# Kernel tuning notes

Hardware: AMD Instinct MI355X
Metric: run time of the kernel (lower is better)

Reference implementation:

```python
import jax, jax.numpy as jnp
import numpy as np
from jax import lax

INF = 1e10
R = 20          # max_distance: EDT truncated at this radius (exact under clamp)
NUM_CLASSES = 19


def _pass1d(f, axis):
    """1D squared distance transform min_{|d|<=R} (d^2 + f[shifted]), truncated.
    f: [..., H, W] with 0 at 'source' pixels, INF elsewhere. Out-of-bounds = INF
    (matches scipy, which sees nothing beyond the array border)."""
    pad = [(0, 0)] * f.ndim
    pad[axis] = (R, R)
    fp = jnp.pad(f, pad, constant_values=INF)
    n = f.shape[axis]
    out = jnp.full_like(f, INF)
    for d in range(2 * R + 1):  # fixed small loop (41 iters), jit-unrolled
        shifted = lax.slice_in_dim(fp, d, d + n, axis=axis)
        out = jnp.minimum(out, shifted + float((d - R) ** 2))
    return out


def edt_trunc(mask):
    """Euclidean distance from each True pixel to nearest False pixel,
    truncated at R (False pixels get 0). mask: [..., H, W] bool."""
    f = jnp.where(mask, INF, 0.0).astype(jnp.float32)
    g = _pass1d(f, -2)
    g = _pass1d(g, -1)
    return jnp.sqrt(jnp.minimum(g, float(R * R)))


def compute_sdf(onehot_bool):
    """Signed distance: negdist - posdist, per [B,C,H,W] one-hot masks.
    Already truncated at +-R, matching clamp(-R, R) in the torch module."""
    posdist = edt_trunc(onehot_bool)    # distance inside FG to BG
    negdist = edt_trunc(~onehot_bool)   # distance inside BG to FG
    return negdist - posdist


def setup_inputs() -> dict:
    key = jax.random.key(0)
    k1, k2 = jax.random.split(key)
    logits = jax.random.normal(k1, (8, NUM_CLASSES, 256, 512), dtype=jnp.float32)
    targets = jax.random.randint(k2, (8, 256, 512), 0, NUM_CLASSES, dtype=jnp.int64)
    return {"logits": logits, "targets": targets}


def reference(logits, targets):
    C = logits.shape[1]
    probs = jax.nn.softmax(logits, axis=1)                       # [B,C,H,W]
    onehot = jax.nn.one_hot(targets, C, axis=1, dtype=jnp.bool_)  # [B,C,H,W]
    sdf = compute_sdf(onehot)
    sdf = jnp.clip(sdf, -float(R), float(R)) / float(R)
    # mean over spatial, sum over classes, mean over batch (reduction='mean')
    per_class = jnp.mean(probs * sdf, axis=(2, 3))               # [B,C]
    loss = jnp.sum(per_class, axis=1)                            # [B]
    return jnp.mean(loss)
```

## Files before the change

kernel.cpp:

```cpp
#include <hip/hip_runtime.h>
#include <hip/hip_bf16.h>
#include <math.h>

#define NCLS 19
#define BB   8
#define HH   256
#define WW   512
#define CAP2 400u
#define SEG  4

typedef unsigned short u16x2 __attribute__((ext_vector_type(2)));

static __device__ __forceinline__ unsigned umin32(unsigned a, unsigned b) { return a < b ? a : b; }
static __device__ __forceinline__ float fsqrt_fast(float x) { return __builtin_amdgcn_sqrtf(x); }

static __device__ __forceinline__ unsigned pk_add_s(unsigned v, unsigned c) {
    unsigned d; asm("v_pk_add_u16 %0, %1, %2" : "=v"(d) : "s"(c), "v"(v)); return d;
}
static __device__ __forceinline__ unsigned pk_minv(unsigned a, unsigned b) {
    unsigned d; asm("v_pk_min_u16 %0, %1, %2" : "=v"(d) : "v"(a), "v"(b)); return d;
}
static __device__ __forceinline__ unsigned pk_maxv(unsigned a, unsigned b) {
    unsigned d; asm("v_pk_max_u16 %0, %1, %2" : "=v"(d) : "v"(a), "v"(b)); return d;
}
static __device__ __forceinline__ unsigned pk_hmin(unsigned a) {
    unsigned d;
    asm("v_pk_min_u16 %0, %1, %1 op_sel:[1,0] op_sel_hi:[0,1]" : "=v"(d) : "v"(a));
    return d;
}
static __device__ __forceinline__ void sq8(unsigned x, unsigned& w0, unsigned& w1) {
    unsigned a = x & 0x00FF00FFu;
    unsigned b = (x >> 8) & 0x00FF00FFu;
    u16x2 sa = __builtin_bit_cast(u16x2, a); sa = sa * sa;
    u16x2 sb = __builtin_bit_cast(u16x2, b); sb = sb * sb;
    unsigned ua = __builtin_bit_cast(unsigned, sa);
    unsigned ub = __builtin_bit_cast(unsigned, sb);
    w0 = __builtin_amdgcn_perm(ub, ua, 0x05040100u);
    w1 = __builtin_amdgcn_perm(ub, ua, 0x07060302u);
}

__global__ __launch_bounds__(256)
void kA_vert(const int* __restrict__ targ, unsigned char* __restrict__ vneg,
             unsigned long long* __restrict__ acc) {
    if (blockIdx.x == 0 && threadIdx.x == 0) { *acc = 0ULL; }
    int gid = blockIdx.x * 256 + threadIdx.x;
    int col = gid & 4095;
    int seg = gid >> 12;
    int b = col >> 9;
    int w = col & 511;
    int h0 = seg * SEG;
    const int* tp = &targ[b * HH * WW + w];

    unsigned d[NCLS], pk[NCLS];
#pragma unroll
    for (int c = 0; c < NCLS; ++c) { d[c] = 21u; pk[c] = 0u; }
#pragma unroll
    for (int k = 0; k < 21 + SEG; ++k) {
        int hh = h0 - 21 + k;
        int t = -1;
        if (hh >= 0) t = tp[hh * WW];
#pragma unroll
        for (int c = 0; c < NCLS; ++c)
            d[c] = (t == c) ? 0u : d[c] + 1u;
        if (k >= 21) {
            int r = k - 21;
#pragma unroll
            for (int c = 0; c < NCLS; ++c)
                pk[c] |= d[c] << (r * 8);
        }
    }
    unsigned u[NCLS];
#pragma unroll
    for (int c = 0; c < NCLS; ++c) u[c] = 21u;
#pragma unroll
    for (int k = 0; k < 21 + SEG; ++k) {
        int hh = h0 + SEG - 1 + 21 - k;
        int t = -1;
        if (hh < HH) t = tp[hh * WW];
#pragma unroll
        for (int c = 0; c < NCLS; ++c)
            u[c] = (t == c) ? 0u : u[c] + 1u;
        if (k >= 21) {
            int r = SEG - 1 - (k - 21);
#pragma unroll
            for (int c = 0; c < NCLS; ++c) {
                unsigned dv = (pk[c] >> (r * 8)) & 0xffu;
                vneg[((size_t)(b * NCLS + c) * HH + (h0 + r)) * WW + w] =
                    (unsigned char)umin32(dv, u[c]);
            }
        }
    }
}

__global__ __launch_bounds__(256)
void kB_main(const float* __restrict__ logits, const int* __restrict__ targ,
             const unsigned char* __restrict__ vneg,
             unsigned long long* __restrict__ acc) {
    __shared__ float sNum[4][256];
    __shared__ float sDen[4][256];
    __shared__ float sEt[4][256];
    __shared__ unsigned short sM2[4][256];
    __shared__ float wsum[4];
    int tid = threadIdx.x;
    int L = tid & 63;
    int wid = tid >> 6;
    int bh = blockIdx.x;
    int b = bh >> 8;
    int h = bh & 255;

    const unsigned HALO2 = 441u | (441u << 16);

#define SQx(x) ((unsigned)((x) * (x)))
#define PK2(a, bq) (SQx(a) | (SQx(bq) << 16))
    const unsigned CE[21] = {
        PK2(-20,-19), PK2(-18,-17), PK2(-16,-15), PK2(-14,-13), PK2(-12,-11),
        PK2(-10,-9),  PK2(-8,-7),   PK2(-6,-5),   PK2(-4,-3),   PK2(-2,-1),
        PK2(0,1),     PK2(2,3),     PK2(4,5),     PK2(6,7),     PK2(8,9),
        PK2(10,11),   PK2(12,13),   PK2(14,15),   PK2(16,17),   PK2(18,19),
        PK2(20,21) };
    const unsigned CO[21] = {
        PK2(-21,-20), PK2(-19,-18), PK2(-17,-16), PK2(-15,-14), PK2(-13,-12),
        PK2(-11,-10), PK2(-9,-8),   PK2(-7,-6),   PK2(-5,-4),   PK2(-3,-2),
        PK2(-1,0),    PK2(1,2),     PK2(3,4),     PK2(5,6),     PK2(7,8),
        PK2(9,10),    PK2(11,12),   PK2(13,14),   PK2(15,16),   PK2(17,18),
        PK2(19,20) };
#undef PK2
#undef SQx

    int im1 = ((L + 63) & 63) * 4, im2 = ((L + 62) & 63) * 4, im3 = ((L + 61) & 63) * 4;
    int ip1 = ((L + 1) & 63) * 4,  ip2 = ((L + 2) & 63) * 4,  ip3 = ((L + 3) & 63) * 4;

    const uint2* vrw = (const uint2*)vneg + ((size_t)(b * NCLS + wid) * HH + h) * 64 + L;
    const float* lroww = &logits[((size_t)(b * NCLS + wid) * HH + h) * WW + 8 * L];
    int nc = (wid < 3) ? 5 : 4;

    int t8[8];
    {
        const int4* tr = (const int4*)&targ[((size_t)b * HH + h) * WW + 8 * L];
        int4 ta = tr[0], tb = tr[1];
        t8[0]=ta.x; t8[1]=ta.y; t8[2]=ta.z; t8[3]=ta.w;
        t8[4]=tb.x; t8[5]=tb.y; t8[6]=tb.z; t8[7]=tb.w;
    }

    float den[8], num[8], et[8];
    unsigned m2[8];
#pragma unroll
    for (int p = 0; p < 8; ++p) { den[p]=0.f; num[p]=0.f; et[p]=0.f; m2[p]=0xFFFFu; }

    uint2 v8n = vrw[0];
    float4 f0n = *(const float4*)lroww;
    float4 f1n = *(const float4*)(lroww + 4);

#pragma unroll 1
    for (int i = 0; i < nc; ++i) {
        int c = wid + 4 * i;
        uint2 v8 = v8n;
        float4 f0 = f0n, f1 = f1n;
        if (i + 1 < nc) {
            size_t off = (size_t)(i + 1) * 4 * (HH * 64);
            v8n = vrw[off];
            const float* ln = lroww + (size_t)(i + 1) * 4 * (HH * WW);
            f0n = *(const float4*)ln;
            f1n = *(const float4*)(ln + 4);
        }

        unsigned o0, o1, o2, o3;
        sq8(v8.x, o0, o1);
        sq8(v8.y, o2, o3);

        unsigned S[24];
        S[10] = o0; S[11] = o1; S[12] = o2; S[13] = o3;
        unsigned t;
        t = __builtin_amdgcn_ds_bpermute(im1, (int)o3); S[9]  = (L >= 1) ? t : HALO2;
        t = __builtin_amdgcn_ds_bpermute(im1, (int)o2); S[8]  = (L >= 1) ? t : HALO2;
        t = __builtin_amdgcn_ds_bpermute(im1, (int)o1); S[7]  = (L >= 1) ? t : HALO2;
        t = __builtin_amdgcn_ds_bpermute(im1, (int)o0); S[6]  = (L >= 1) ? t : HALO2;
        t = __builtin_amdgcn_ds_bpermute(im2, (int)o3); S[5]  = (L >= 2) ? t : HALO2;
        t = __builtin_amdgcn_ds_bpermute(im2, (int)o2); S[4]  = (L >= 2) ? t : HALO2;
        t = __builtin_amdgcn_ds_bpermute(im2, (int)o1); S[3]  = (L >= 2) ? t : HALO2;
        t = __builtin_amdgcn_ds_bpermute(im2, (int)o0); S[2]  = (L >= 2) ? t : HALO2;
        t = __builtin_amdgcn_ds_bpermute(im3, (int)o3); S[1]  = (L >= 3) ? t : HALO2;
        t = __builtin_amdgcn_ds_bpermute(im3, (int)o2); S[0]  = (L >= 3) ? t : HALO2;
        t = __builtin_amdgcn_ds_bpermute(ip1, (int)o0); S[14] = (L <= 62) ? t : HALO2;
        t = __builtin_amdgcn_ds_bpermute(ip1, (int)o1); S[15] = (L <= 62) ? t : HALO2;
        t = __builtin_amdgcn_ds_bpermute(ip1, (int)o2); S[16] = (L <= 62) ? t : HALO2;
        t = __builtin_amdgcn_ds_bpermute(ip1, (int)o3); S[17] = (L <= 62) ? t : HALO2;
        t = __builtin_amdgcn_ds_bpermute(ip2, (int)o0); S[18] = (L <= 61) ? t : HALO2;
        t = __builtin_amdgcn_ds_bpermute(ip2, (int)o1); S[19] = (L <= 61) ? t : HALO2;
        t = __builtin_amdgcn_ds_bpermute(ip2, (int)o2); S[20] = (L <= 61) ? t : HALO2;
        t = __builtin_amdgcn_ds_bpermute(ip2, (int)o3); S[21] = (L <= 61) ? t : HALO2;
        t = __builtin_amdgcn_ds_bpermute(ip3, (int)o0); S[22] = (L <= 60) ? t : HALO2;
        t = __builtin_amdgcn_ds_bpermute(ip3, (int)o1); S[23] = (L <= 60) ? t : HALO2;

        unsigned ae[4], ao[4];
#pragma unroll
        for (int r = 0; r < 4; ++r) { ae[r] = 0xFFFFFFFFu; ao[r] = 0xFFFFFFFFu; }

#pragma unroll
        for (int r = 0; r < 4; ++r)
#pragma unroll
            for (int m = 7; m <= 13; ++m) {
                ae[r] = pk_minv(ae[r], pk_add_s(S[r + m], CE[m]));
                ao[r] = pk_minv(ao[r], pk_add_s(S[r + m], CO[m]));
            }

        unsigned mx = pk_maxv(pk_maxv(pk_maxv(pk_hmin(ae[0]), pk_hmin(ao[0])),
                                      pk_maxv(pk_hmin(ae[1]), pk_hmin(ao[1]))),
                              pk_maxv(pk_maxv(pk_hmin(ae[2]), pk_hmin(ao[2])),
                                      pk_maxv(pk_hmin(ae[3]), pk_hmin(ao[3]))));
        if (!__all(mx <= (49u | (49u << 16)))) {
#pragma unroll
            for (int r = 0; r < 4; ++r) {
#pragma unroll
                for (int m = 4; m <= 6; ++m) {
                    ae[r] = pk_minv(ae[r], pk_add_s(S[r + m], CE[m]));
                    ao[r] = pk_minv(ao[r], pk_add_s(S[r + m], CO[m]));
                }
#pragma unroll
                for (int m = 14; m <= 16; ++m) {
                    ae[r] = pk_minv(ae[r], pk_add_s(S[r + m], CE[m]));
                    ao[r] = pk_minv(ao[r], pk_add_s(S[r + m], CO[m]));
                }
            }
            mx = pk_maxv(pk_maxv(pk_maxv(pk_hmin(ae[0]), pk_hmin(ao[0])),
                                 pk_maxv(pk_hmin(ae[1]), pk_hmin(ao[1]))),
                         pk_maxv(pk_maxv(pk_hmin(ae[2]), pk_hmin(ao[2])),
                                 pk_maxv(pk_hmin(ae[3]), pk_hmin(ao[3]))));
            if (!__all(mx <= (169u | (169u << 16)))) {
#pragma unroll
                for (int r = 0; r < 4; ++r) {
#pragma unroll
                    for (int m = 0; m <= 3; ++m) {
                        ae[r] = pk_minv(ae[r], pk_add_s(S[r + m], CE[m]));
                        ao[r] = pk_minv(ao[r], pk_add_s(S[r + m], CO[m]));
                    }
#pragma unroll
                    for (int m = 17; m <= 20; ++m) {
                        ae[r] = pk_minv(ae[r], pk_add_s(S[r + m], CE[m]));
                        ao[r] = pk_minv(ao[r], pk_add_s(S[r + m], CO[m]));
                    }
                }
            }
        }

        float fx[8] = {f0.x, f0.y, f0.z, f0.w, f1.x, f1.y, f1.z, f1.w};
#pragma unroll
        for (int r = 0; r < 4; ++r) {
            unsigned nd0 = pk_hmin(ae[r]) & 0xFFFFu;
            unsigned nd1 = pk_hmin(ao[r]) & 0xFFFFu;
            float e0 = __expf(fx[2 * r]), e1 = __expf(fx[2 * r + 1]);
            den[2 * r] += e0; den[2 * r + 1] += e1;
            bool is0 = (c == t8[2 * r]), is1 = (c == t8[2 * r + 1]);
            float s0 = fsqrt_fast((float)umin32(nd0, CAP2));
            float s1 = fsqrt_fast((float)umin32(nd1, CAP2));
            num[2 * r]     += is0 ? 0.f : e0 * s0;
            num[2 * r + 1] += is1 ? 0.f : e1 * s1;
            et[2 * r]     = is0 ? e0 : et[2 * r];
            et[2 * r + 1] = is1 ? e1 : et[2 * r + 1];
            m2[2 * r]     = umin32(m2[2 * r],     is0 ? 0xFFFFu : nd0);
            m2[2 * r + 1] = umin32(m2[2 * r + 1], is1 ? 0xFFFFu : nd1);
        }
    }

    float vsum = 0.f;
#pragma unroll
    for (int pass = 0; pass < 2; ++pass) {
        if ((L >> 5) == pass) {
            int base = 8 * (L & 31);
            *(float4*)&sNum[wid][base]     = (float4){num[0], num[1], num[2], num[3]};
            *(float4*)&sNum[wid][base + 4] = (float4){num[4], num[5], num[6], num[7]};
            *(float4*)&sDen[wid][base]     = (float4){den[0], den[1], den[2], den[3]};
            *(float4*)&sDen[wid][base + 4] = (float4){den[4], den[5], den[6], den[7]};
            *(float4*)&sEt[wid][base]      = (float4){et[0], et[1], et[2], et[3]};
            *(float4*)&sEt[wid][base + 4]  = (float4){et[4], et[5], et[6], et[7]};
            uint4 mq;
            mq.x = m2[0] | (m2[1] << 16); mq.y = m2[2] | (m2[3] << 16);
            mq.z = m2[4] | (m2[5] << 16); mq.w = m2[6] | (m2[7] << 16);
            *(uint4*)&sM2[wid][base] = mq;
        }
        __syncthreads();
        {
            float N = sNum[0][tid] + sNum[1][tid] + sNum[2][tid] + sNum[3][tid];
            float D = sDen[0][tid] + sDen[1][tid] + sDen[2][tid] + sDen[3][tid];
            float E = sEt[0][tid] + sEt[1][tid] + sEt[2][tid] + sEt[3][tid];
            unsigned M = umin32(umin32((unsigned)sM2[0][tid], (unsigned)sM2[1][tid]),
                                umin32((unsigned)sM2[2][tid], (unsigned)sM2[3][tid]));
            vsum += (N - E * fsqrt_fast((float)umin32(M, CAP2))) / D;
        }
        __syncthreads();
    }

#pragma unroll
    for (int off = 32; off >= 1; off >>= 1) vsum += __shfl_down(vsum, off);
    if (L == 0) wsum[wid] = vsum;
    __syncthreads();
    if (tid == 0) {
        float s = (wsum[0] + wsum[1]) + (wsum[2] + wsum[3]);
        double q = (double)s * (68719476736.0 / 20.0);
        atomicAdd(acc, (unsigned long long)(long long)q);
    }
}

__global__ void kC_final(const unsigned long long* __restrict__ acc,
                         float* __restrict__ out) {
    long long iv = (long long)*acc;
    double v = (double)iv / 68719476736.0;
    out[0] = (float)(v / (double)((size_t)BB * HH * WW));
}

extern "C" void kernel_launch(void* const* d_in, const int* in_sizes, int n_in,
                              void* d_out, int out_size, void* d_ws, size_t ws_size,
                              hipStream_t stream) {
    const float* logits = (const float*)d_in[0];
    const int* targ = (const int*)d_in[1];
    unsigned char* wsb = (unsigned char*)d_ws;
    unsigned long long* acc = (unsigned long long*)wsb;
    unsigned char* vneg = wsb + 64;

    kA_vert<<<1024, 256, 0, stream>>>(targ, vneg, acc);
    kB_main<<<BB * HH, 256, 0, stream>>>(logits, targ, vneg, acc);
    kC_final<<<1, 1, 0, stream>>>(acc, (float*)d_out);
}
```

Measured before the change: 66.15 us.

## Double kA segment length, drop target reads in kB, merge EDT tail stages

The vertical-distance kernel now handles 8 rows per thread instead of 4, halving its grid and cutting the redundant halo scans, and keeps two packed words per class. The main kernel no longer reads targets; it infers class membership from a zero vertical distance, which saves one row read per block. The two-level early-exit for wider horizontal windows becomes a single fallback that scans the full window, and an occupancy hint is added to the launch bounds. This trades fewer loads and wave votes for more min ops in rare blocks and higher register pressure in kA.

```diff
diff --git a/kernel.cpp b/kernel.cpp
--- a/kernel.cpp
+++ b/kernel.cpp
@@ -7,7 +7,7 @@
 #define HH   256
 #define WW   512
 #define CAP2 400u
-#define SEG  4
+#define SEG  8
 
 typedef unsigned short u16x2 __attribute__((ext_vector_type(2)));
 
@@ -51,9 +51,10 @@
     int h0 = seg * SEG;
     const int* tp = &targ[b * HH * WW + w];
 
-    unsigned d[NCLS], pk[NCLS];
-#pragma unroll
-    for (int c = 0; c < NCLS; ++c) { d[c] = 21u; pk[c] = 0u; }
+    unsigned d[NCLS];
+    unsigned pk[NCLS][2];
+#pragma unroll
+    for (int c = 0; c < NCLS; ++c) { d[c] = 21u; pk[c][0] = 0u; pk[c][1] = 0u; }
 #pragma unroll
     for (int k = 0; k < 21 + SEG; ++k) {
         int hh = h0 - 21 + k;
@@ -66,7 +67,7 @@
             int r = k - 21;
 #pragma unroll
             for (int c = 0; c < NCLS; ++c)
-                pk[c] |= d[c] << (r * 8);
+                pk[c][r >> 2] |= d[c] << ((r & 3) * 8);
         }
     }
     unsigned u[NCLS];
@@ -74,26 +75,26 @@
     for (int c = 0; c < NCLS; ++c) u[c] = 21u;
 #pragma unroll
     for (int k = 0; k < 21 + SEG; ++k) {
-        int hh = h0 + SEG - 1 + 21 - k;
+        int hh = h0 + 21 + SEG - 1 - k;
         int t = -1;
         if (hh < HH) t = tp[hh * WW];
 #pragma unroll
         for (int c = 0; c < NCLS; ++c)
             u[c] = (t == c) ? 0u : u[c] + 1u;
         if (k >= 21) {
-            int r = SEG - 1 - (k - 21);
+            int r = 21 + SEG - 1 - k;
 #pragma unroll
             for (int c = 0; c < NCLS; ++c) {
-                unsigned dv = (pk[c] >> (r * 8)) & 0xffu;
-                vneg[((size_t)(b * NCLS + c) * HH + (h0 + r)) * WW + w] =
+                unsigned dv = (pk[c][r >> 2] >> ((r & 3) * 8)) & 0xffu;
+                vneg[((size_t)(b * NCLS + c) * HH + hh) * WW + w] =
                     (unsigned char)umin32(dv, u[c]);
             }
         }
     }
 }
 
-__global__ __launch_bounds__(256)
-void kB_main(const float* __restrict__ logits, const int* __restrict__ targ,
+__global__ __launch_bounds__(256, 8)
+void kB_main(const float* __restrict__ logits,
              const unsigned char* __restrict__ vneg,
              unsigned long long* __restrict__ acc) {
     __shared__ float sNum[4][256];
@@ -134,14 +135,6 @@
     const float* lroww = &logits[((size_t)(b * NCLS + wid) * HH + h) * WW + 8 * L];
     int nc = (wid < 3) ? 5 : 4;
 
-    int t8[8];
-    {
-        const int4* tr = (const int4*)&targ[((size_t)b * HH + h) * WW + 8 * L];
-        int4 ta = tr[0], tb = tr[1];
-        t8[0]=ta.x; t8[1]=ta.y; t8[2]=ta.z; t8[3]=ta.w;
-        t8[4]=tb.x; t8[5]=tb.y; t8[6]=tb.z; t8[7]=tb.w;
-    }
-
     float den[8], num[8], et[8];
     unsigned m2[8];
 #pragma unroll
@@ -153,7 +146,6 @@
 
 #pragma unroll 1
     for (int i = 0; i < nc; ++i) {
-        int c = wid + 4 * i;
         uint2 v8 = v8n;
         float4 f0 = f0n, f1 = f1n;
         if (i + 1 < nc) {
@@ -212,33 +204,14 @@
 #pragma unroll
             for (int r = 0; r < 4; ++r) {
 #pragma unroll
-                for (int m = 4; m <= 6; ++m) {
+                for (int m = 0; m <= 6; ++m) {
                     ae[r] = pk_minv(ae[r], pk_add_s(S[r + m], CE[m]));
                     ao[r] = pk_minv(ao[r], pk_add_s(S[r + m], CO[m]));
                 }
 #pragma unroll
-                for (int m = 14; m <= 16; ++m) {
+                for (int m = 14; m <= 20; ++m) {
                     ae[r] = pk_minv(ae[r], pk_add_s(S[r + m], CE[m]));
                     ao[r] = pk_minv(ao[r], pk_add_s(S[r + m], CO[m]));
-                }
-            }
-            mx = pk_maxv(pk_maxv(pk_maxv(pk_hmin(ae[0]), pk_hmin(ao[0])),
-                                 pk_maxv(pk_hmin(ae[1]), pk_hmin(ao[1]))),
-                         pk_maxv(pk_maxv(pk_hmin(ae[2]), pk_hmin(ao[2])),
-                                 pk_maxv(pk_hmin(ae[3]), pk_hmin(ao[3]))));
-            if (!__all(mx <= (169u | (169u << 16)))) {
-#pragma unroll
-                for (int r = 0; r < 4; ++r) {
-#pragma unroll
-                    for (int m = 0; m <= 3; ++m) {
-                        ae[r] = pk_minv(ae[r], pk_add_s(S[r + m], CE[m]));
-                        ao[r] = pk_minv(ao[r], pk_add_s(S[r + m], CO[m]));
-                    }
-#pragma unroll
-                    for (int m = 17; m <= 20; ++m) {
-                        ae[r] = pk_minv(ae[r], pk_add_s(S[r + m], CE[m]));
-                        ao[r] = pk_minv(ao[r], pk_add_s(S[r + m], CO[m]));
-                    }
                 }
             }
         }
@@ -250,15 +223,15 @@
             unsigned nd1 = pk_hmin(ao[r]) & 0xFFFFu;
             float e0 = __expf(fx[2 * r]), e1 = __expf(fx[2 * r + 1]);
             den[2 * r] += e0; den[2 * r + 1] += e1;
-            bool is0 = (c == t8[2 * r]), is1 = (c == t8[2 * r + 1]);
             float s0 = fsqrt_fast((float)umin32(nd0, CAP2));
             float s1 = fsqrt_fast((float)umin32(nd1, CAP2));
-            num[2 * r]     += is0 ? 0.f : e0 * s0;
-            num[2 * r + 1] += is1 ? 0.f : e1 * s1;
-            et[2 * r]     = is0 ? e0 : et[2 * r];
-            et[2 * r + 1] = is1 ? e1 : et[2 * r + 1];
-            m2[2 * r]     = umin32(m2[2 * r],     is0 ? 0xFFFFu : nd0);
-            m2[2 * r + 1] = umin32(m2[2 * r + 1], is1 ? 0xFFFFu : nd1);
+            num[2 * r]     += e0 * s0;
+            num[2 * r + 1] += e1 * s1;
+            bool z0 = (nd0 == 0), z1 = (nd1 == 0);
+            et[2 * r]     = z0 ? e0 : et[2 * r];
+            et[2 * r + 1] = z1 ? e1 : et[2 * r + 1];
+            m2[2 * r]     = umin32(m2[2 * r],     z0 ? 0xFFFFu : nd0);
+            m2[2 * r + 1] = umin32(m2[2 * r + 1], z1 ? 0xFFFFu : nd1);
         }
     }
 
@@ -317,7 +290,7 @@
     unsigned long long* acc = (unsigned long long*)wsb;
     unsigned char* vneg = wsb + 64;
 
-    kA_vert<<<1024, 256, 0, stream>>>(targ, vneg, acc);
-    kB_main<<<BB * HH, 256, 0, stream>>>(logits, targ, vneg, acc);
+    kA_vert<<<512, 256, 0, stream>>>(targ, vneg, acc);
+    kB_main<<<BB * HH, 256, 0, stream>>>(logits, vneg, acc);
     kC_final<<<1, 1, 0, stream>>>(acc, (float*)d_out);
 }
```

Measured after the change: 138.5 us. +109.4%, slower.
